# Optimization experiments

Measured on AMD Instinct MI355X. Metric: run time of the kernel, lower is better.

Reference implementation:

```python
import jax, jax.numpy as jnp
import numpy as np

N_NODES = 50000
N_EDGES = 800000
HEADS = 4
HID = 48
NEG_SLOPE = 0.2


def setup_inputs() -> dict:
    key = jax.random.key(0)
    ks = list(jax.random.split(key, 32))
    inp = {}
    inp['x'] = jax.random.normal(ks[0], (N_NODES, 3), dtype=jnp.float32)
    inp['edge_index'] = jax.random.randint(ks[1], (2, N_EDGES), 0, N_NODES, dtype=jnp.int64)
    dims = [3, HID, HID]
    ki = 2
    for li, din in enumerate(dims):
        s = 1.0 / np.sqrt(din)
        inp[f'Wl{li}'] = jax.random.normal(ks[ki], (din, HEADS * HID), dtype=jnp.float32) * s; ki += 1
        inp[f'bl{li}'] = jnp.zeros((HEADS * HID,), dtype=jnp.float32)
        inp[f'Wr{li}'] = jax.random.normal(ks[ki], (din, HEADS * HID), dtype=jnp.float32) * s; ki += 1
        inp[f'br{li}'] = jnp.zeros((HEADS * HID,), dtype=jnp.float32)
        inp[f'att{li}'] = jax.random.normal(ks[ki], (HEADS, HID), dtype=jnp.float32) * (1.0 / np.sqrt(HID)); ki += 1
        inp[f'bias{li}'] = jnp.zeros((HID,), dtype=jnp.float32)
    inp['head_w'] = jax.random.normal(ks[ki], (HID, 1), dtype=jnp.float32) * (1.0 / np.sqrt(HID))
    inp['head_b'] = jnp.full((1,), 0.1, dtype=jnp.float32)
    return inp


def _gatv2_layer(x, src, dst, Wl, bl, Wr, br, att, bias):
    # GATv2Conv, concat=False, eval mode (dropout off), self-loops already in (src,dst)
    N = x.shape[0]
    xl = (x @ Wl + bl).reshape(N, HEADS, HID)  # source transform
    xr = (x @ Wr + br).reshape(N, HEADS, HID)  # target transform
    e = jax.nn.leaky_relu(xl[src] + xr[dst], NEG_SLOPE)  # [E,H,C]
    score = jnp.einsum('ehc,hc->eh', e, att)             # [E,H]
    # segment softmax over edges grouped by destination node
    m = jax.ops.segment_max(score, dst, num_segments=N)
    p = jnp.exp(score - m[dst])
    denom = jax.ops.segment_sum(p, dst, num_segments=N)
    alpha = p / (denom[dst] + 1e-16)                     # [E,H]
    out = jax.ops.segment_sum(alpha[..., None] * xl[src], dst, num_segments=N)  # [N,H,C]
    return out.mean(axis=1) + bias  # concat=False -> mean over heads


def reference(x, edge_index, Wl0, bl0, Wr0, br0, att0, bias0,
              Wl1, bl1, Wr1, br1, att1, bias1,
              Wl2, bl2, Wr2, br2, att2, bias2, head_w, head_b):
    N = x.shape[0]
    loops = jnp.arange(N, dtype=edge_index.dtype)
    src = jnp.concatenate([edge_index[0], loops])  # PyG add_self_loops=True
    dst = jnp.concatenate([edge_index[1], loops])
    params = [(Wl0, bl0, Wr0, br0, att0, bias0),
              (Wl1, bl1, Wr1, br1, att1, bias1),
              (Wl2, bl2, Wr2, br2, att2, bias2)]
    for (Wl, bl, Wr, br, att, bias) in params:
        x = _gatv2_layer(x, src, dst, Wl, bl, Wr, br, att, bias)
        x = jax.nn.elu(x)
    out = (x @ head_w + head_b)[:, 0]
    return jax.nn.relu(out)
```

## Files before the change

### kernel.cpp

```cpp
#include <hip/hip_runtime.h>
#include <hip/hip_bf16.h>
#include <math.h>

#define HEADS 4
#define HID 48
#define FDIM 192
#define NEG_SLOPE 0.2f

typedef float f4 __attribute__((ext_vector_type(4)));

template<int CTRL>
__device__ __forceinline__ float dpp_add(float v) {
    int t = __builtin_amdgcn_update_dpp(0, __float_as_int(v), CTRL, 0xF, 0xF, true);
    return v + __int_as_float(t);
}
__device__ __forceinline__ float red16(float v) {
    v = dpp_add<0xB1>(v);
    v = dpp_add<0x4E>(v);
    v = dpp_add<0x124>(v);
    v = dpp_add<0x128>(v);
    return v;
}

__device__ __forceinline__ int detect64(const int* __restrict__ ei) {
    int l = (int)(threadIdx.x & 63);
    int v = ei[2 * l + 1];
    return (__ballot(v != 0) == 0ULL) ? 1 : 0;
}

__global__ void hist_kernel(const int* __restrict__ ei,
                            int* __restrict__ deg, int E, int E2) {
    int is64 = detect64(ei);
    for (int e = blockIdx.x * blockDim.x + threadIdx.x; e < E2;
         e += gridDim.x * blockDim.x) {
        int d;
        if (e < E) d = is64 ? ei[2 * (E + e)] : ei[E + e];
        else       d = e - E;
        atomicAdd(&deg[d], 1);
    }
}

__global__ void scan_local_kernel(const int* __restrict__ deg, int* __restrict__ incl,
                                  int* __restrict__ bsum, int N) {
    __shared__ int sm[256];
    int i = blockIdx.x * 256 + threadIdx.x;
    int v = (i < N) ? deg[i] : 0;
    sm[threadIdx.x] = v;
    __syncthreads();
    #pragma unroll
    for (int off = 1; off < 256; off <<= 1) {
        int t = ((int)threadIdx.x >= off) ? sm[threadIdx.x - off] : 0;
        __syncthreads();
        sm[threadIdx.x] += t;
        __syncthreads();
    }
    if (i < N) incl[i] = sm[threadIdx.x];
    if (threadIdx.x == 255) bsum[blockIdx.x] = sm[255];
}

__global__ void scan_bsum_kernel(int* __restrict__ bsum, int nb) {
    __shared__ int sm[256];
    __shared__ int running;
    if (threadIdx.x == 0) running = 0;
    __syncthreads();
    for (int base = 0; base < nb; base += 256) {
        int i = base + (int)threadIdx.x;
        int v = (i < nb) ? bsum[i] : 0;
        sm[threadIdx.x] = v;
        __syncthreads();
        #pragma unroll
        for (int off = 1; off < 256; off <<= 1) {
            int t = ((int)threadIdx.x >= off) ? sm[threadIdx.x - off] : 0;
            __syncthreads();
            sm[threadIdx.x] += t;
            __syncthreads();
        }
        if (i < nb) bsum[i] = running + sm[threadIdx.x] - v;
        __syncthreads();
        if (threadIdx.x == 0) running += sm[255];
        __syncthreads();
    }
}

__global__ void scan_final_kernel(const int* __restrict__ incl, const int* __restrict__ bsum,
                                  int* __restrict__ rowptr, int* __restrict__ cursor, int N) {
    int i = blockIdx.x * 256 + threadIdx.x;
    if (i < N) { rowptr[i + 1] = incl[i] + bsum[blockIdx.x]; cursor[i] = 0; }
    if (i == 0) rowptr[0] = 0;
}

__global__ void scatter_kernel(const int* __restrict__ ei,
                               const int* __restrict__ rowptr, int* __restrict__ cursor,
                               int* __restrict__ srcs, int E, int E2) {
    int is64 = detect64(ei);
    for (int e = blockIdx.x * blockDim.x + threadIdx.x; e < E2;
         e += gridDim.x * blockDim.x) {
        int s, d;
        if (e < E) {
            if (is64) { s = ei[2 * e]; d = ei[2 * (E + e)]; }
            else      { s = ei[e];     d = ei[E + e]; }
        } else {
            s = d = e - E;
        }
        int pos = rowptr[d] + atomicAdd(&cursor[d], 1);
        srcs[pos] = s;
    }
}

template<int DIN>
__global__ __launch_bounds__(192) void gemm2t_kernel(
    const float* __restrict__ xin,
    const float* __restrict__ Wl, const float* __restrict__ bl,
    const float* __restrict__ Wr, const float* __restrict__ br,
    float* __restrict__ xl, float* __restrict__ xr, int N) {
    int t  = (int)threadIdx.x;
    int cg = t % 48;
    int ng = t / 48;
    int c0 = cg * 4;
    int n0 = blockIdx.x * 16 + ng * 4;
    if (n0 >= N) return;

    f4 bLv = *(const f4*)&bl[c0];
    f4 bRv = *(const f4*)&br[c0];
    f4 accL[4], accR[4];
    #pragma unroll
    for (int i = 0; i < 4; ++i) { accL[i] = bLv; accR[i] = bRv; }

    if (n0 + 3 < N) {
        if (DIN == 3) {
            float xv[4][3];
            #pragma unroll
            for (int i = 0; i < 4; ++i) {
                const float* xp = xin + (size_t)(n0 + i) * 3;
                xv[i][0] = xp[0]; xv[i][1] = xp[1]; xv[i][2] = xp[2];
            }
            #pragma unroll
            for (int k = 0; k < 3; ++k) {
                f4 wl4 = *(const f4*)&Wl[k * FDIM + c0];
                f4 wr4 = *(const f4*)&Wr[k * FDIM + c0];
                #pragma unroll
                for (int i = 0; i < 4; ++i) {
                    float xs = xv[i][k];
                    accL[i] += xs * wl4;
                    accR[i] += xs * wr4;
                }
            }
        } else {
            #pragma unroll
            for (int kk = 0; kk < DIN; kk += 8) {
                float xv[4][8];
                #pragma unroll
                for (int i = 0; i < 4; ++i) {
                    const float* xp = xin + (size_t)(n0 + i) * DIN + kk;
                    f4 xa = *(const f4*)xp;
                    f4 xb = *(const f4*)(xp + 4);
                    #pragma unroll
                    for (int q = 0; q < 4; ++q) { xv[i][q] = xa[q]; xv[i][4 + q] = xb[q]; }
                }
                #pragma unroll
                for (int k = 0; k < 8; ++k) {
                    f4 wl4 = *(const f4*)&Wl[(kk + k) * FDIM + c0];
                    f4 wr4 = *(const f4*)&Wr[(kk + k) * FDIM + c0];
                    #pragma unroll
                    for (int i = 0; i < 4; ++i) {
                        float xs = xv[i][k];
                        accL[i] += xs * wl4;
                        accR[i] += xs * wr4;
                    }
                }
            }
        }
        #pragma unroll
        for (int i = 0; i < 4; ++i) {
            *(f4*)&xl[(size_t)(n0 + i) * FDIM + c0] = accL[i];
            *(f4*)&xr[(size_t)(n0 + i) * FDIM + c0] = accR[i];
        }
    } else {
        for (int i = 0; i < 4; ++i) {
            int n = n0 + i;
            if (n >= N) break;
            f4 aL = bLv;
            f4 aR = bRv;
            for (int k = 0; k < DIN; ++k) {
                float xs = xin[(size_t)n * DIN + k];
                f4 wl4 = *(const f4*)&Wl[k * FDIM + c0];
                f4 wr4 = *(const f4*)&Wr[k * FDIM + c0];
                aL += xs * wl4;
                aR += xs * wr4;
            }
            *(f4*)&xl[(size_t)n * FDIM + c0] = aL;
            *(f4*)&xr[(size_t)n * FDIM + c0] = aR;
        }
    }
}

#define SCORE_MASKED (-1e38f)
#define M_INIT       (-3e38f)
#define DEFER_THR    8.0f

__global__ __launch_bounds__(256) void gat_layer_kernel(
    const float* __restrict__ xl, const float* __restrict__ xr,
    const float* __restrict__ att, const float* __restrict__ bias,
    const int* __restrict__ rowptr, const int* __restrict__ srcs,
    float* __restrict__ xout,
    float* __restrict__ out,
    const float* __restrict__ head_w, const float* __restrict__ head_b,
    int N, int final_flag) {
    int wave = (int)((blockIdx.x * blockDim.x + threadIdx.x) >> 6);
    wave = __builtin_amdgcn_readfirstlane(wave);
    if (wave >= N) return;
    int lane = (int)(threadIdx.x & 63);
    int n  = wave;
    int h  = lane >> 4;
    int cl = lane & 15;
    int j0 = h * HID + cl;

    float a0 = att[j0], a1 = att[j0 + 16], a2 = att[j0 + 32];
    const float* xrp = xr + (size_t)n * FDIM;
    float r0 = xrp[j0], r1 = xrp[j0 + 16], r2 = xrp[j0 + 32];

    float m = M_INIT, denom = 0.f;
    float acc0 = 0.f, acc1 = 0.f, acc2 = 0.f;

    int e0 = rowptr[n], e1 = rowptr[n + 1];
    int elast = e1 - 1;

    for (int e = e0; e < e1; e += 4) {
        int i0 = e,     i1 = e + 1,  i2 = e + 2,  i3 = e + 3;
        int k0 = (i0 < e1) ? i0 : elast;
        int k1 = (i1 < e1) ? i1 : elast;
        int k2 = (i2 < e1) ? i2 : elast;
        int k3 = (i3 < e1) ? i3 : elast;
        int s0 = srcs[k0], s1 = srcs[k1], s2 = srcs[k2], s3 = srcs[k3];
        const float* p0 = xl + (size_t)s0 * FDIM;
        const float* p1 = xl + (size_t)s1 * FDIM;
        const float* p2 = xl + (size_t)s2 * FDIM;
        const float* p3 = xl + (size_t)s3 * FDIM;
        float l00 = p0[j0], l01 = p0[j0 + 16], l02 = p0[j0 + 32];
        float l10 = p1[j0], l11 = p1[j0 + 16], l12 = p1[j0 + 32];
        float l20 = p2[j0], l21 = p2[j0 + 16], l22 = p2[j0 + 32];
        float l30 = p3[j0], l31 = p3[j0 + 16], l32 = p3[j0 + 32];

        #define LRELU(x) (fmaf(NEG_SLOPE, fminf((x), 0.f), fmaxf((x), 0.f)))
        float sc0 = LRELU(l00 + r0) * a0 + LRELU(l01 + r1) * a1 + LRELU(l02 + r2) * a2;
        float sc1 = LRELU(l10 + r0) * a0 + LRELU(l11 + r1) * a1 + LRELU(l12 + r2) * a2;
        float sc2 = LRELU(l20 + r0) * a0 + LRELU(l21 + r1) * a1 + LRELU(l22 + r2) * a2;
        float sc3 = LRELU(l30 + r0) * a0 + LRELU(l31 + r1) * a1 + LRELU(l32 + r2) * a2;
        #undef LRELU
        sc0 = red16(sc0); sc1 = red16(sc1); sc2 = red16(sc2); sc3 = red16(sc3);
        sc0 = (i0 < e1) ? sc0 : SCORE_MASKED;
        sc1 = (i1 < e1) ? sc1 : SCORE_MASKED;
        sc2 = (i2 < e1) ? sc2 : SCORE_MASKED;
        sc3 = (i3 < e1) ? sc3 : SCORE_MASKED;

        float bmax = fmaxf(fmaxf(sc0, sc1), fmaxf(sc2, sc3));
        if (__any(bmax > m + DEFER_THR)) {
            float nm = fmaxf(m, bmax);
            float sc = __expf(m - nm);
            denom *= sc; acc0 *= sc; acc1 *= sc; acc2 *= sc;
            m = nm;
        }
        float q0 = __expf(sc0 - m);
        float q1 = __expf(sc1 - m);
        float q2 = __expf(sc2 - m);
        float q3 = __expf(sc3 - m);
        denom += (q0 + q1) + (q2 + q3);
        acc0 = fmaf(q0, l00, fmaf(q1, l10, fmaf(q2, l20, fmaf(q3, l30, acc0))));
        acc1 = fmaf(q0, l01, fmaf(q1, l11, fmaf(q2, l21, fmaf(q3, l31, acc1))));
        acc2 = fmaf(q0, l02, fmaf(q1, l12, fmaf(q2, l22, fmaf(q3, l32, acc2))));
    }

    float inv = 1.0f / (denom + 1e-16f);
    float o0 = acc0 * inv, o1 = acc1 * inv, o2 = acc2 * inv;
    o0 += __shfl_xor(o0, 16); o0 += __shfl_xor(o0, 32);
    o1 += __shfl_xor(o1, 16); o1 += __shfl_xor(o1, 32);
    o2 += __shfl_xor(o2, 16); o2 += __shfl_xor(o2, 32);
    o0 = 0.25f * o0 + bias[cl];
    o1 = 0.25f * o1 + bias[cl + 16];
    o2 = 0.25f * o2 + bias[cl + 32];
    o0 = (o0 > 0.f) ? o0 : expm1f(o0);
    o1 = (o1 > 0.f) ? o1 : expm1f(o1);
    o2 = (o2 > 0.f) ? o2 : expm1f(o2);

    if (!final_flag) {
        if (h == 0) {
            float* xo = xout + (size_t)n * HID;
            xo[cl] = o0; xo[cl + 16] = o1; xo[cl + 32] = o2;
        }
    } else {
        float part = o0 * head_w[cl] + o1 * head_w[cl + 16] + o2 * head_w[cl + 32];
        part = red16(part);
        if (lane == 0) {
            float v = part + head_b[0];
            out[n] = (v > 0.f) ? v : 0.f;
        }
    }
}

extern "C" void kernel_launch(void* const* d_in, const int* in_sizes, int n_in,
                              void* d_out, int out_size, void* d_ws, size_t ws_size,
                              hipStream_t stream) {
    const float* x0 = (const float*)d_in[0];
    const int*   ei = (const int*)d_in[1];

    const int N  = in_sizes[0] / 3;
    const int E  = in_sizes[1] / 2;
    const int E2 = E + N;

    const float* Wl[3];  const float* bl[3];
    const float* Wr[3];  const float* br[3];
    const float* att[3]; const float* bias[3];
    for (int li = 0; li < 3; ++li) {
        int b = 2 + 6 * li;
        Wl[li]   = (const float*)d_in[b + 0];
        bl[li]   = (const float*)d_in[b + 1];
        Wr[li]   = (const float*)d_in[b + 2];
        br[li]   = (const float*)d_in[b + 3];
        att[li]  = (const float*)d_in[b + 4];
        bias[li] = (const float*)d_in[b + 5];
    }
    const float* head_w = (const float*)d_in[20];
    const float* head_b = (const float*)d_in[21];
    float* out = (float*)d_out;

    size_t off = 0;
    auto alloc = [&](size_t bytes) -> void* {
        void* p = (char*)d_ws + off;
        off = (off + bytes + 255) & ~(size_t)255;
        return p;
    };
    const int nb = (N + 255) / 256;
    int*   deg    = (int*)alloc((size_t)N * sizeof(int));
    int*   incl   = (int*)alloc((size_t)N * sizeof(int));
    int*   bsum   = (int*)alloc((size_t)nb * sizeof(int));
    int*   rowptr = (int*)alloc((size_t)(N + 1) * sizeof(int));
    int*   srcs   = (int*)alloc((size_t)E2 * sizeof(int));
    float* xlb    = (float*)alloc((size_t)N * FDIM * sizeof(float));
    float* xrb    = (float*)alloc((size_t)N * FDIM * sizeof(float));
    float* xbuf   = (float*)alloc((size_t)N * HID * sizeof(float));
    (void)ws_size;

    (void)hipMemsetAsync(deg, 0, (size_t)N * sizeof(int), stream);
    hist_kernel<<<2048, 256, 0, stream>>>(ei, deg, E, E2);
    scan_local_kernel<<<nb, 256, 0, stream>>>(deg, incl, bsum, N);
    scan_bsum_kernel<<<1, 256, 0, stream>>>(bsum, nb);
    scan_final_kernel<<<nb, 256, 0, stream>>>(incl, bsum, rowptr, deg, N);
    scatter_kernel<<<2048, 256, 0, stream>>>(ei, rowptr, deg, srcs, E, E2);

    const int waves_per_block = 4;
    int gat_blocks = (N + waves_per_block - 1) / waves_per_block;
    int gemm_blocks = (N + 15) / 16;

    gemm2t_kernel<3><<<gemm_blocks, 192, 0, stream>>>(x0, Wl[0], bl[0], Wr[0], br[0], xlb, xrb, N);
    gat_layer_kernel<<<gat_blocks, 256, 0, stream>>>(xlb, xrb, att[0], bias[0],
        rowptr, srcs, xbuf, nullptr, nullptr, nullptr, N, 0);

    gemm2t_kernel<HID><<<gemm_blocks, 192, 0, stream>>>(xbuf, Wl[1], bl[1], Wr[1], br[1], xlb, xrb, N);
    gat_layer_kernel<<<gat_blocks, 256, 0, stream>>>(xlb, xrb, att[1], bias[1],
        rowptr, srcs, xbuf, nullptr, nullptr, nullptr, N, 0);

    gemm2t_kernel<HID><<<gemm_blocks, 192, 0, stream>>>(xbuf, Wl[2], bl[2], Wr[2], br[2], xlb, xrb, N);
    gat_layer_kernel<<<gat_blocks, 256, 0, stream>>>(xlb, xrb, att[2], bias[2],
        rowptr, srcs, nullptr, out, head_w, head_b, N, 1);

    (void)n_in; (void)out_size;
}
```

Measured before the change: 480.0 us.

## Remap GAT lanes to 4 edge slots by 4 channel quads with float4 gathers

The aggregation kernel's lane mapping changes from 16 lanes per head each holding 3 strided channels to 4 edge slots times 4 channel groups of 12 contiguous channels. Each lane now gathers its xl row slice with 128-bit vector loads and processes 8 edges per iteration, two per lane. Per-edge score reduction shrinks to a 4-lane DPP sum, and a cross-slot max and final accumulator reduction are added. The aim is fewer, wider gather transactions and more edges in flight, at the cost of extra reductions and more registers for the float4 accumulators.

```diff
diff --git a/kernel.cpp b/kernel.cpp
--- a/kernel.cpp
+++ b/kernel.cpp
@@ -14,11 +14,24 @@
     int t = __builtin_amdgcn_update_dpp(0, __float_as_int(v), CTRL, 0xF, 0xF, true);
     return v + __int_as_float(t);
 }
-__device__ __forceinline__ float red16(float v) {
+template<int CTRL>
+__device__ __forceinline__ float dpp_max(float v) {
+    int t = __builtin_amdgcn_update_dpp(0, __float_as_int(v), CTRL, 0xF, 0xF, true);
+    return fmaxf(v, __int_as_float(t));
+}
+__device__ __forceinline__ float red_cq(float v) {
     v = dpp_add<0xB1>(v);
     v = dpp_add<0x4E>(v);
+    return v;
+}
+__device__ __forceinline__ float red_es(float v) {
     v = dpp_add<0x124>(v);
     v = dpp_add<0x128>(v);
+    return v;
+}
+__device__ __forceinline__ float rowmax16(float v) {
+    v = dpp_max<0x124>(v);
+    v = dpp_max<0x128>(v);
     return v;
 }
 
@@ -212,84 +225,115 @@
     int lane = (int)(threadIdx.x & 63);
     int n  = wave;
     int h  = lane >> 4;
-    int cl = lane & 15;
-    int j0 = h * HID + cl;
-
-    float a0 = att[j0], a1 = att[j0 + 16], a2 = att[j0 + 32];
-    const float* xrp = xr + (size_t)n * FDIM;
-    float r0 = xrp[j0], r1 = xrp[j0 + 16], r2 = xrp[j0 + 32];
-
-    float m = M_INIT, denom = 0.f;
-    float acc0 = 0.f, acc1 = 0.f, acc2 = 0.f;
+    int es = (lane >> 2) & 3;
+    int cq = lane & 3;
+    int j0 = h * HID + cq * 12;
+
+    const float* xrp = xr + (size_t)n * FDIM + j0;
+    f4 r0 = *(const f4*)xrp;
+    f4 r1 = *(const f4*)(xrp + 4);
+    f4 r2 = *(const f4*)(xrp + 8);
+    f4 a0 = *(const f4*)&att[j0];
+    f4 a1 = *(const f4*)&att[j0 + 4];
+    f4 a2 = *(const f4*)&att[j0 + 8];
+
+    float m = M_INIT, dn = 0.f;
+    f4 acc0 = {0.f, 0.f, 0.f, 0.f}, acc1 = acc0, acc2 = acc0;
 
     int e0 = rowptr[n], e1 = rowptr[n + 1];
     int elast = e1 - 1;
 
-    for (int e = e0; e < e1; e += 4) {
-        int i0 = e,     i1 = e + 1,  i2 = e + 2,  i3 = e + 3;
-        int k0 = (i0 < e1) ? i0 : elast;
-        int k1 = (i1 < e1) ? i1 : elast;
-        int k2 = (i2 < e1) ? i2 : elast;
-        int k3 = (i3 < e1) ? i3 : elast;
-        int s0 = srcs[k0], s1 = srcs[k1], s2 = srcs[k2], s3 = srcs[k3];
-        const float* p0 = xl + (size_t)s0 * FDIM;
-        const float* p1 = xl + (size_t)s1 * FDIM;
-        const float* p2 = xl + (size_t)s2 * FDIM;
-        const float* p3 = xl + (size_t)s3 * FDIM;
-        float l00 = p0[j0], l01 = p0[j0 + 16], l02 = p0[j0 + 32];
-        float l10 = p1[j0], l11 = p1[j0 + 16], l12 = p1[j0 + 32];
-        float l20 = p2[j0], l21 = p2[j0 + 16], l22 = p2[j0 + 32];
-        float l30 = p3[j0], l31 = p3[j0 + 16], l32 = p3[j0 + 32];
-
-        #define LRELU(x) (fmaf(NEG_SLOPE, fminf((x), 0.f), fmaxf((x), 0.f)))
-        float sc0 = LRELU(l00 + r0) * a0 + LRELU(l01 + r1) * a1 + LRELU(l02 + r2) * a2;
-        float sc1 = LRELU(l10 + r0) * a0 + LRELU(l11 + r1) * a1 + LRELU(l12 + r2) * a2;
-        float sc2 = LRELU(l20 + r0) * a0 + LRELU(l21 + r1) * a1 + LRELU(l22 + r2) * a2;
-        float sc3 = LRELU(l30 + r0) * a0 + LRELU(l31 + r1) * a1 + LRELU(l32 + r2) * a2;
-        #undef LRELU
-        sc0 = red16(sc0); sc1 = red16(sc1); sc2 = red16(sc2); sc3 = red16(sc3);
-        sc0 = (i0 < e1) ? sc0 : SCORE_MASKED;
-        sc1 = (i1 < e1) ? sc1 : SCORE_MASKED;
-        sc2 = (i2 < e1) ? sc2 : SCORE_MASKED;
-        sc3 = (i3 < e1) ? sc3 : SCORE_MASKED;
-
-        float bmax = fmaxf(fmaxf(sc0, sc1), fmaxf(sc2, sc3));
+    for (int e = e0; e < e1; e += 8) {
+        int iA = e + es;
+        int iB = e + 4 + es;
+        int kA = (iA < e1) ? iA : elast;
+        int kB = (iB < e1) ? iB : elast;
+        int sA = srcs[kA];
+        int sB = srcs[kB];
+        const float* pA = xl + (size_t)sA * FDIM + j0;
+        const float* pB = xl + (size_t)sB * FDIM + j0;
+        f4 A0 = *(const f4*)pA, A1 = *(const f4*)(pA + 4), A2 = *(const f4*)(pA + 8);
+        f4 B0 = *(const f4*)pB, B1 = *(const f4*)(pB + 4), B2 = *(const f4*)(pB + 8);
+
+        float scA = 0.f, scB = 0.f;
+        #pragma unroll
+        for (int q = 0; q < 4; ++q) {
+            float t, u;
+            t = A0[q] + r0[q]; u = fmaf(NEG_SLOPE, fminf(t, 0.f), fmaxf(t, 0.f)); scA = fmaf(u, a0[q], scA);
+            t = A1[q] + r1[q]; u = fmaf(NEG_SLOPE, fminf(t, 0.f), fmaxf(t, 0.f)); scA = fmaf(u, a1[q], scA);
+            t = A2[q] + r2[q]; u = fmaf(NEG_SLOPE, fminf(t, 0.f), fmaxf(t, 0.f)); scA = fmaf(u, a2[q], scA);
+            t = B0[q] + r0[q]; u = fmaf(NEG_SLOPE, fminf(t, 0.f), fmaxf(t, 0.f)); scB = fmaf(u, a0[q], scB);
+            t = B1[q] + r1[q]; u = fmaf(NEG_SLOPE, fminf(t, 0.f), fmaxf(t, 0.f)); scB = fmaf(u, a1[q], scB);
+            t = B2[q] + r2[q]; u = fmaf(NEG_SLOPE, fminf(t, 0.f), fmaxf(t, 0.f)); scB = fmaf(u, a2[q], scB);
+        }
+        scA = red_cq(scA);
+        scB = red_cq(scB);
+        scA = (iA < e1) ? scA : SCORE_MASKED;
+        scB = (iB < e1) ? scB : SCORE_MASKED;
+
+        float bmax = rowmax16(fmaxf(scA, scB));
         if (__any(bmax > m + DEFER_THR)) {
             float nm = fmaxf(m, bmax);
-            float sc = __expf(m - nm);
-            denom *= sc; acc0 *= sc; acc1 *= sc; acc2 *= sc;
+            float sc_ = __expf(m - nm);
+            dn *= sc_; acc0 *= sc_; acc1 *= sc_; acc2 *= sc_;
             m = nm;
         }
-        float q0 = __expf(sc0 - m);
-        float q1 = __expf(sc1 - m);
-        float q2 = __expf(sc2 - m);
-        float q3 = __expf(sc3 - m);
-        denom += (q0 + q1) + (q2 + q3);
-        acc0 = fmaf(q0, l00, fmaf(q1, l10, fmaf(q2, l20, fmaf(q3, l30, acc0))));
-        acc1 = fmaf(q0, l01, fmaf(q1, l11, fmaf(q2, l21, fmaf(q3, l31, acc1))));
-        acc2 = fmaf(q0, l02, fmaf(q1, l12, fmaf(q2, l22, fmaf(q3, l32, acc2))));
-    }
-
-    float inv = 1.0f / (denom + 1e-16f);
-    float o0 = acc0 * inv, o1 = acc1 * inv, o2 = acc2 * inv;
-    o0 += __shfl_xor(o0, 16); o0 += __shfl_xor(o0, 32);
-    o1 += __shfl_xor(o1, 16); o1 += __shfl_xor(o1, 32);
-    o2 += __shfl_xor(o2, 16); o2 += __shfl_xor(o2, 32);
-    o0 = 0.25f * o0 + bias[cl];
-    o1 = 0.25f * o1 + bias[cl + 16];
-    o2 = 0.25f * o2 + bias[cl + 32];
-    o0 = (o0 > 0.f) ? o0 : expm1f(o0);
-    o1 = (o1 > 0.f) ? o1 : expm1f(o1);
-    o2 = (o2 > 0.f) ? o2 : expm1f(o2);
+        float qA = __expf(scA - m);
+        float qB = __expf(scB - m);
+        dn += qA + qB;
+        acc0 += qA * A0 + qB * B0;
+        acc1 += qA * A1 + qB * B1;
+        acc2 += qA * A2 + qB * B2;
+    }
+
+    dn = red_es(dn);
+    #pragma unroll
+    for (int q = 0; q < 4; ++q) {
+        acc0[q] = red_es(acc0[q]);
+        acc1[q] = red_es(acc1[q]);
+        acc2[q] = red_es(acc2[q]);
+    }
+
+    float inv = 1.0f / (dn + 1e-16f);
+    f4 o0 = acc0 * inv, o1 = acc1 * inv, o2 = acc2 * inv;
+
+    #pragma unroll
+    for (int q = 0; q < 4; ++q) {
+        float v;
+        v = o0[q]; v += __shfl_xor(v, 16); v += __shfl_xor(v, 32); o0[q] = v;
+        v = o1[q]; v += __shfl_xor(v, 16); v += __shfl_xor(v, 32); o1[q] = v;
+        v = o2[q]; v += __shfl_xor(v, 16); v += __shfl_xor(v, 32); o2[q] = v;
+    }
+    int c0 = cq * 12;
+    f4 b0v = *(const f4*)&bias[c0];
+    f4 b1v = *(const f4*)&bias[c0 + 4];
+    f4 b2v = *(const f4*)&bias[c0 + 8];
+    o0 = 0.25f * o0 + b0v;
+    o1 = 0.25f * o1 + b1v;
+    o2 = 0.25f * o2 + b2v;
+    #pragma unroll
+    for (int q = 0; q < 4; ++q) {
+        o0[q] = (o0[q] > 0.f) ? o0[q] : (__expf(o0[q]) - 1.f);
+        o1[q] = (o1[q] > 0.f) ? o1[q] : (__expf(o1[q]) - 1.f);
+        o2[q] = (o2[q] > 0.f) ? o2[q] : (__expf(o2[q]) - 1.f);
+    }
 
     if (!final_flag) {
-        if (h == 0) {
-            float* xo = xout + (size_t)n * HID;
-            xo[cl] = o0; xo[cl + 16] = o1; xo[cl + 32] = o2;
+        if (h == 0 && es == 0) {
+            float* xo = xout + (size_t)n * HID + c0;
+            *(f4*)xo = o0;
+            *(f4*)(xo + 4) = o1;
+            *(f4*)(xo + 8) = o2;
         }
     } else {
-        float part = o0 * head_w[cl] + o1 * head_w[cl + 16] + o2 * head_w[cl + 32];
-        part = red16(part);
+        f4 w0 = *(const f4*)&head_w[c0];
+        f4 w1 = *(const f4*)&head_w[c0 + 4];
+        f4 w2 = *(const f4*)&head_w[c0 + 8];
+        float part = 0.f;
+        #pragma unroll
+        for (int q = 0; q < 4; ++q)
+            part += o0[q] * w0[q] + o1[q] * w1[q] + o2[q] * w2[q];
+        part = red_cq(part);
         if (lane == 0) {
             float v = part + head_b[0];
             out[n] = (v > 0.f) ? v : 0.f;
```

New measurement: 490.2 us. 2.1% more time.
